# Kernel tuning notes

Measured on AMD Instinct MI355X. Metric: run time of the kernel, lower is better.

Reference implementation:

```python
import jax, jax.numpy as jnp
import numpy as np

OFFSETS = list(range(0, 8))  # s_prev=0, s_curr=7 -> kernel_size K=8
NEG = -1e9  # finite stand-in for -inf in masked softmax (avoids NaN rows)


def setup_inputs() -> dict:
    key = jax.random.key(0)
    ks = jax.random.split(key, 5)
    B, N, d = 8, 4096, 256
    x = jax.random.normal(ks[0], (B, N, d), dtype=jnp.float32)
    # most-recent-first: index 0 has smallest time delta -> sorted ascending
    delta_times = jnp.sort(jax.random.uniform(ks[1], (B, N), dtype=jnp.float32) * 100.0, axis=1)
    lengths = jax.random.randint(ks[2], (B,), N // 2, N + 1)
    valid_mask = jnp.arange(N)[None, :] < lengths[:, None]  # [B, N] bool
    w = jax.random.normal(ks[3], (len(OFFSETS),), dtype=jnp.float32) * 0.1
    beta = jax.random.normal(ks[4], (1,), dtype=jnp.float32) * 0.1
    return {"x": x, "delta_times": delta_times, "valid_mask": valid_mask, "w": w, "beta": beta}


def _mixer(x, delta_times, valid_mask, w, beta):
    B, N, d = x.shape
    sxs, tds, cvs = [], [], []
    for p in OFFSETS:  # small fixed kernel window, K=8
        if p == 0:
            sxs.append(x)
            tds.append(jnp.zeros((B, N), x.dtype))
            cvs.append(valid_mask)
        else:
            sxs.append(jnp.pad(x[:, p:], ((0, 0), (0, p), (0, 0))))
            tds.append(jnp.pad(jnp.maximum(delta_times[:, p:] - delta_times[:, :N - p], 0.0), ((0, 0), (0, p))))
            cvs.append(jnp.pad(valid_mask[:, p:] & valid_mask[:, :N - p], ((0, 0), (0, p))))
    sx = jnp.stack(sxs, axis=2)  # [B, N, K, d]
    td = jnp.stack(tds, axis=2)  # [B, N, K]
    cv = jnp.stack(cvs, axis=2)  # [B, N, K] bool
    # temporal-decay softmax over offsets (masked positions -> ~0 weight)
    theta = jax.nn.softmax(jnp.where(cv, -td, NEG), axis=2)
    wsm = jax.nn.softmax(w)[None, None, :]  # learnable per-offset weights
    b = jax.nn.sigmoid(beta[0])
    alpha = jnp.where(cv, b * wsm + (1.0 - b) * theta, 0.0)
    alpha = alpha / jnp.maximum(alpha.sum(axis=2, keepdims=True), 1e-8)
    out = jnp.einsum('bnkd,bnk->bnd', sx, alpha)
    return out * valid_mask[..., None].astype(x.dtype)


def reference(x, delta_times, valid_mask, w, beta):
    # Dropout is identity in eval mode.
    return _mixer(x, delta_times, valid_mask, w, beta)
```

## Files before the change

### kernel.cpp

```cpp
#include <hip/hip_runtime.h>


#define NEGV (-1e9f)

constexpr int Bc = 8;
constexpr int Nc = 4096;
constexpr int D4 = 64;
constexpr int Kc = 8;
constexpr int Tr = 32;
constexpr int XR = Tr + Kc - 1;

__global__ __launch_bounds__(256) void atm_kernel(
    const float* __restrict__ x,
    const float* __restrict__ dt,
    const void* __restrict__ maskp,
    const float* __restrict__ w,
    const float* __restrict__ beta,
    float* __restrict__ out)
{
    __shared__ float4 xs[XR * D4];
    __shared__ float alphas[Tr][Kc];

    const int tid = threadIdx.x;
    const int tiles_per_b = Nc / Tr;
    const int b = blockIdx.x / tiles_per_b;
    const int n0 = (blockIdx.x % tiles_per_b) * Tr;
    const long row0 = (long)b * Nc + n0;

    const float4* __restrict__ x4 = (const float4*)x;
    const long total4 = (long)Bc * Nc * D4;
    const long base4 = row0 * D4;
#pragma unroll
    for (int i = tid; i < XR * D4; i += 256) {
        const long g = base4 + i;
        xs[i] = (g < total4) ? x4[g] : make_float4(0.f, 0.f, 0.f, 0.f);
    }

    {
        const int r = tid >> 3;
        const int p = tid & 7;
        const int n = n0 + r;
        const long rowm = row0 + r;

        const unsigned char* m8 = (const unsigned char*)maskp;
        const int* m32 = (const int*)maskp;
        const bool is_byte = (m8[1] != 0);
        auto getm = [&](long i) -> bool {
            return is_byte ? (m8[i] != 0) : (m32[i] != 0);
        };

        bool c;
        float td = 0.f;
        if (p == 0) {
            c = getm(rowm);
        } else if (n + p < Nc) {
            c = getm(rowm) && getm(rowm + p);
            td = fmaxf(dt[rowm + p] - dt[rowm], 0.f);
        } else {
            c = false;
        }
        const float lg = c ? -td : NEGV;

        float mx = lg;
        mx = fmaxf(mx, __shfl_xor(mx, 1));
        mx = fmaxf(mx, __shfl_xor(mx, 2));
        mx = fmaxf(mx, __shfl_xor(mx, 4));
        const float th = expf(lg - mx);
        float tsum = th;
        tsum += __shfl_xor(tsum, 1);
        tsum += __shfl_xor(tsum, 2);
        tsum += __shfl_xor(tsum, 4);

        const float wv = w[p];
        float wmax = wv;
        wmax = fmaxf(wmax, __shfl_xor(wmax, 1));
        wmax = fmaxf(wmax, __shfl_xor(wmax, 2));
        wmax = fmaxf(wmax, __shfl_xor(wmax, 4));
        const float we = expf(wv - wmax);
        float wsum = we;
        wsum += __shfl_xor(wsum, 1);
        wsum += __shfl_xor(wsum, 2);
        wsum += __shfl_xor(wsum, 4);

        const float bsig = 1.0f / (1.0f + expf(-beta[0]));
        const float a = c ? (bsig * we / wsum + (1.0f - bsig) * th / tsum) : 0.f;
        float asum = a;
        asum += __shfl_xor(asum, 1);
        asum += __shfl_xor(asum, 2);
        asum += __shfl_xor(asum, 4);
        alphas[r][p] = a / fmaxf(asum, 1e-8f);
    }

    __syncthreads();

    const int wave = tid >> 6;
    const int lane = tid & 63;
    float4* __restrict__ out4 = (float4*)out;
#pragma unroll
    for (int rr = 0; rr < 8; ++rr) {
        const int r = wave * 8 + rr;
        float4 acc = make_float4(0.f, 0.f, 0.f, 0.f);
#pragma unroll
        for (int p = 0; p < Kc; ++p) {
            const float a = alphas[r][p];
            const float4 xv = xs[(r + p) * D4 + lane];
            acc.x = fmaf(a, xv.x, acc.x);
            acc.y = fmaf(a, xv.y, acc.y);
            acc.z = fmaf(a, xv.z, acc.z);
            acc.w = fmaf(a, xv.w, acc.w);
        }
        out4[(row0 + r) * D4 + lane] = acc;
    }
}

extern "C" void kernel_launch(void* const* d_in, const int* in_sizes, int n_in,
                              void* d_out, int out_size, void* d_ws, size_t ws_size,
                              hipStream_t stream) {
    const float* x    = (const float*)d_in[0];
    const float* dt   = (const float*)d_in[1];
    const void*  mask = d_in[2];
    const float* w    = (const float*)d_in[3];
    const float* beta = (const float*)d_in[4];
    float* out = (float*)d_out;

    dim3 grid(Bc * Nc / Tr);
    dim3 block(256);
    atm_kernel<<<grid, block, 0, stream>>>(x, dt, mask, w, beta, out);
}
```

Measured before the change: 93.30 us.

## Replace shared-memory tile with per-wave register window and shuffled alphas

Each wave now independently processes 8 rows, loading a 15-row x window directly into registers and broadcasting per-row alpha weights via lane shuffles instead of LDS. This removes shared memory usage and the block-wide barrier, letting waves proceed independently. It trades this for more redundant global reads of overlapping halo rows (15 loads per 8 outputs versus 39 per 32), relying on L2 to absorb the overlap, and increases register pressure.

After: 91.50 us. About the same (-1.9%).

```diff
diff --git a/kernel.cpp b/kernel.cpp
--- a/kernel.cpp
+++ b/kernel.cpp
@@ -6,9 +6,8 @@
 constexpr int Bc = 8;
 constexpr int Nc = 4096;
 constexpr int D4 = 64;
-constexpr int Kc = 8;
-constexpr int Tr = 32;
-constexpr int XR = Tr + Kc - 1;
+constexpr int Rw = 8;
+constexpr int XR = 15;
 
 __global__ __launch_bounds__(256) void atm_kernel(
     const float* __restrict__ x,
@@ -18,96 +17,87 @@
     const float* __restrict__ beta,
     float* __restrict__ out)
 {
-    __shared__ float4 xs[XR * D4];
-    __shared__ float alphas[Tr][Kc];
-
     const int tid = threadIdx.x;
-    const int tiles_per_b = Nc / Tr;
-    const int b = blockIdx.x / tiles_per_b;
-    const int n0 = (blockIdx.x % tiles_per_b) * Tr;
+    const int lane = tid & 63;
+    const int gw = blockIdx.x * 4 + (tid >> 6);
+    const int waves_per_b = Nc / Rw;
+    const int b = gw / waves_per_b;
+    const int n0 = (gw % waves_per_b) * Rw;
     const long row0 = (long)b * Nc + n0;
 
+    const int r_l = lane >> 3;
+    const int p_l = lane & 7;
+    const int n = n0 + r_l;
+    const long rowm = row0 + r_l;
+
+    const unsigned char* m8 = (const unsigned char*)maskp;
+    const int* m32 = (const int*)maskp;
+    const bool is_byte = (m8[1] != 0);
+    auto getm = [&](long i) -> bool {
+        return is_byte ? (m8[i] != 0) : (m32[i] != 0);
+    };
+
+    bool c;
+    float td = 0.f;
+    if (p_l == 0) {
+        c = getm(rowm);
+    } else if (n + p_l < Nc) {
+        c = getm(rowm) && getm(rowm + p_l);
+        td = fmaxf(dt[rowm + p_l] - dt[rowm], 0.f);
+    } else {
+        c = false;
+    }
+    const float lg = c ? -td : NEGV;
+
+    float mx = lg;
+    mx = fmaxf(mx, __shfl_xor(mx, 1));
+    mx = fmaxf(mx, __shfl_xor(mx, 2));
+    mx = fmaxf(mx, __shfl_xor(mx, 4));
+    const float th = expf(lg - mx);
+    float tsum = th;
+    tsum += __shfl_xor(tsum, 1);
+    tsum += __shfl_xor(tsum, 2);
+    tsum += __shfl_xor(tsum, 4);
+
+    const float wv = w[p_l];
+    float wmax = wv;
+    wmax = fmaxf(wmax, __shfl_xor(wmax, 1));
+    wmax = fmaxf(wmax, __shfl_xor(wmax, 2));
+    wmax = fmaxf(wmax, __shfl_xor(wmax, 4));
+    const float we = expf(wv - wmax);
+    float wsum = we;
+    wsum += __shfl_xor(wsum, 1);
+    wsum += __shfl_xor(wsum, 2);
+    wsum += __shfl_xor(wsum, 4);
+
+    const float bsig = 1.0f / (1.0f + expf(-beta[0]));
+    const float a = c ? (bsig * we / wsum + (1.0f - bsig) * th / tsum) : 0.f;
+    float asum = a;
+    asum += __shfl_xor(asum, 1);
+    asum += __shfl_xor(asum, 2);
+    asum += __shfl_xor(asum, 4);
+    const float aval = a / fmaxf(asum, 1e-8f);
+
     const float4* __restrict__ x4 = (const float4*)x;
-    const long total4 = (long)Bc * Nc * D4;
-    const long base4 = row0 * D4;
+    float4 win[XR];
 #pragma unroll
-    for (int i = tid; i < XR * D4; i += 256) {
-        const long g = base4 + i;
-        xs[i] = (g < total4) ? x4[g] : make_float4(0.f, 0.f, 0.f, 0.f);
+    for (int j = 0; j < XR; ++j) {
+        win[j] = (n0 + j < Nc) ? x4[(row0 + j) * D4 + lane]
+                               : make_float4(0.f, 0.f, 0.f, 0.f);
     }
 
-    {
-        const int r = tid >> 3;
-        const int p = tid & 7;
-        const int n = n0 + r;
-        const long rowm = row0 + r;
-
-        const unsigned char* m8 = (const unsigned char*)maskp;
-        const int* m32 = (const int*)maskp;
-        const bool is_byte = (m8[1] != 0);
-        auto getm = [&](long i) -> bool {
-            return is_byte ? (m8[i] != 0) : (m32[i] != 0);
-        };
-
-        bool c;
-        float td = 0.f;
-        if (p == 0) {
-            c = getm(rowm);
-        } else if (n + p < Nc) {
-            c = getm(rowm) && getm(rowm + p);
-            td = fmaxf(dt[rowm + p] - dt[rowm], 0.f);
-        } else {
-            c = false;
-        }
-        const float lg = c ? -td : NEGV;
-
-        float mx = lg;
-        mx = fmaxf(mx, __shfl_xor(mx, 1));
-        mx = fmaxf(mx, __shfl_xor(mx, 2));
-        mx = fmaxf(mx, __shfl_xor(mx, 4));
-        const float th = expf(lg - mx);
-        float tsum = th;
-        tsum += __shfl_xor(tsum, 1);
-        tsum += __shfl_xor(tsum, 2);
-        tsum += __shfl_xor(tsum, 4);
-
-        const float wv = w[p];
-        float wmax = wv;
-        wmax = fmaxf(wmax, __shfl_xor(wmax, 1));
-        wmax = fmaxf(wmax, __shfl_xor(wmax, 2));
-        wmax = fmaxf(wmax, __shfl_xor(wmax, 4));
-        const float we = expf(wv - wmax);
-        float wsum = we;
-        wsum += __shfl_xor(wsum, 1);
-        wsum += __shfl_xor(wsum, 2);
-        wsum += __shfl_xor(wsum, 4);
-
-        const float bsig = 1.0f / (1.0f + expf(-beta[0]));
-        const float a = c ? (bsig * we / wsum + (1.0f - bsig) * th / tsum) : 0.f;
-        float asum = a;
-        asum += __shfl_xor(asum, 1);
-        asum += __shfl_xor(asum, 2);
-        asum += __shfl_xor(asum, 4);
-        alphas[r][p] = a / fmaxf(asum, 1e-8f);
-    }
-
-    __syncthreads();
-
-    const int wave = tid >> 6;
-    const int lane = tid & 63;
     float4* __restrict__ out4 = (float4*)out;
 #pragma unroll
-    for (int rr = 0; rr < 8; ++rr) {
-        const int r = wave * 8 + rr;
+    for (int r = 0; r < Rw; ++r) {
         float4 acc = make_float4(0.f, 0.f, 0.f, 0.f);
 #pragma unroll
-        for (int p = 0; p < Kc; ++p) {
-            const float a = alphas[r][p];
-            const float4 xv = xs[(r + p) * D4 + lane];
-            acc.x = fmaf(a, xv.x, acc.x);
-            acc.y = fmaf(a, xv.y, acc.y);
-            acc.z = fmaf(a, xv.z, acc.z);
-            acc.w = fmaf(a, xv.w, acc.w);
+        for (int p = 0; p < 8; ++p) {
+            const float av = __shfl(aval, r * 8 + p);
+            const float4 xv = win[r + p];
+            acc.x = fmaf(av, xv.x, acc.x);
+            acc.y = fmaf(av, xv.y, acc.y);
+            acc.z = fmaf(av, xv.z, acc.z);
+            acc.w = fmaf(av, xv.w, acc.w);
         }
         out4[(row0 + r) * D4 + lane] = acc;
     }
@@ -123,7 +113,7 @@
     const float* beta = (const float*)d_in[4];
     float* out = (float*)d_out;
 
-    dim3 grid(Bc * Nc / Tr);
+    dim3 grid(Bc * Nc / (Rw * 4));
     dim3 block(256);
     atm_kernel<<<grid, block, 0, stream>>>(x, dt, mask, w, beta, out);
 }
```
